# Kernel tuning notes

Measured on AMD Instinct MI355X. Metric: run time of the kernel, lower is better.

The kernel has to match this reference:

```python
import jax, jax.numpy as jnp
import numpy as np

N, IN_DIM, OUT_DIM = 8192, 512, 256
ALPHA = 0.2
NEG_INF = -9e15


def setup_inputs() -> dict:
    key = jax.random.key(0)
    k1, k2, k3, k4 = jax.random.split(key, 4)
    node_features = jax.random.normal(k1, (N, IN_DIM), dtype=jnp.float32)
    adj_matrix = jax.random.randint(k2, (N, N), 0, 2, dtype=jnp.int32)
    # xavier-uniform linear weight [out,in] -> store as [in,out]
    lim_w = float(np.sqrt(6.0 / (IN_DIM + OUT_DIM)))
    W = jax.random.uniform(k3, (IN_DIM, OUT_DIM), dtype=jnp.float32, minval=-lim_w, maxval=lim_w)
    b = jnp.zeros((OUT_DIM,), dtype=jnp.float32)
    # attention Linear(2*out_dim, 1): weight a [2*out_dim], bias scalar
    lim_a = float(np.sqrt(6.0 / (2 * OUT_DIM + 1)))
    a = jax.random.uniform(k4, (2 * OUT_DIM,), dtype=jnp.float32, minval=-lim_a, maxval=lim_a)
    a_bias = jnp.zeros((), dtype=jnp.float32)
    return {"adj_matrix": adj_matrix, "node_features": node_features, "W": W, "b": b, "a": a, "a_bias": a_bias}


def reference(adj_matrix, node_features, W, b, a, a_bias):
    # h = Linear(node_features); dropout is identity in eval mode
    h = node_features @ W + b                     # [N, D]
    # attention(cat(h_i, h_j)) == h_i @ a_l + h_j @ a_r + a_bias
    a_l, a_r = a[:OUT_DIM], a[OUT_DIM:]
    e_l = h @ a_l                                 # [N]
    e_r = h @ a_r                                 # [N]
    e = jax.nn.leaky_relu(e_l[:, None] + e_r[None, :] + a_bias, ALPHA)  # [N, N]
    scores = jnp.where(adj_matrix > 0, e, NEG_INF)
    attention = jax.nn.softmax(scores, axis=1)    # [N, N]
    h_prime = attention @ h                       # [N, D]
    return h_prime
```

## Files before the change

kernel.cpp:

```cpp
#include <hip/hip_runtime.h>

#define N 8192
#define DIN 512
#define DOUT 256
#define ALPHA 0.2f
#define NEG_INF -9.0e15f

typedef __attribute__((ext_vector_type(8))) short bf16x8;
typedef __attribute__((ext_vector_type(4))) float f32x4;
typedef __attribute__((ext_vector_type(4))) int   i32x4;

__device__ __forceinline__ unsigned f2bf_u(float f) {
    unsigned u = __builtin_bit_cast(unsigned, f);
    return (u + 0x7fffu + ((u >> 16) & 1u)) >> 16;
}
__device__ __forceinline__ unsigned pack2bf(float lo, float hi) {
    return f2bf_u(lo) | (f2bf_u(hi) << 16);
}
union U4BF8 { uint4 u; bf16x8 v; };

__device__ __forceinline__ void async_copy16(const ushort* g, ushort* l) {
    __builtin_amdgcn_global_load_lds(
        (const __attribute__((address_space(1))) unsigned*)g,
        (__attribute__((address_space(3))) unsigned*)l, 16, 0, 0);
}

__global__ __launch_bounds__(256) void wb_kernel(const float* __restrict__ W,
                                                 ushort* __restrict__ WB) {
    const int g = blockIdx.x * 256 + threadIdx.x;
    const int c = g & 255, k8 = g >> 8;
    const float* wp = W + (size_t)(k8 * 8) * DOUT + c;
    U4BF8 o;
    o.u.x = pack2bf(wp[0 * DOUT], wp[1 * DOUT]);
    o.u.y = pack2bf(wp[2 * DOUT], wp[3 * DOUT]);
    o.u.z = pack2bf(wp[4 * DOUT], wp[5 * DOUT]);
    o.u.w = pack2bf(wp[6 * DOUT], wp[7 * DOUT]);
    *(uint4*)(WB + (size_t)g * 8) = o.u;
}

__global__ __launch_bounds__(256) void h_kernel(
        const float* __restrict__ X, const ushort* __restrict__ WB,
        const float* __restrict__ bvec, const float* __restrict__ a,
        ushort* __restrict__ hB, float* __restrict__ el, float* __restrict__ er)
{
    __shared__ float red[4][64][65];
    __shared__ float elr[2][4][16];
    const int t = threadIdx.x;
    const int w = t >> 6, l = t & 63, q = l >> 4, n = l & 15;
    const int i0 = blockIdx.x * 16;
    f32x4 acc[16];
    #pragma unroll
    for (int ct = 0; ct < 16; ++ct) acc[ct] = (f32x4){0.f, 0.f, 0.f, 0.f};
    const float* xp = X + (size_t)(i0 + n) * DIN + q * 8;

    #pragma unroll
    for (int ks = 0; ks < 4; ++ks) {
        const int k0 = w * 128 + ks * 32;
        const float4 x0 = *(const float4*)(xp + k0);
        const float4 x1 = *(const float4*)(xp + k0 + 4);
        U4BF8 pa;
        pa.u.x = pack2bf(x0.x, x0.y); pa.u.y = pack2bf(x0.z, x0.w);
        pa.u.z = pack2bf(x1.x, x1.y); pa.u.w = pack2bf(x1.z, x1.w);
        const ushort* wbp = WB + ((k0 >> 3) + q) * 2048 + n * 8;
        bf16x8 bfr[16];
        #pragma unroll
        for (int ct = 0; ct < 16; ++ct) bfr[ct] = *(const bf16x8*)(wbp + ct * 128);
        #pragma unroll
        for (int ct = 0; ct < 16; ++ct)
            acc[ct] = __builtin_amdgcn_mfma_f32_16x16x32_bf16(pa.v, bfr[ct], acc[ct], 0, 0, 0);
    }
    #pragma unroll
    for (int ct = 0; ct < 16; ++ct)
        #pragma unroll
        for (int r = 0; r < 4; ++r) red[w][l][ct * 4 + r] = acc[ct][r];
    __syncthreads();

    float pl[4] = {0.f, 0.f, 0.f, 0.f}, pr[4] = {0.f, 0.f, 0.f, 0.f};
    const int hbase = (blockIdx.x * 2 + (q >> 1)) * 2048 + n * 8 + (q & 1) * 4;
    #pragma unroll
    for (int c2 = 0; c2 < 4; ++c2) {
        const int ct = w * 4 + c2;
        const float bb = bvec[ct * 16 + n];
        const float al = a[ct * 16 + n];
        const float ar = a[DOUT + ct * 16 + n];
        float v[4];
        #pragma unroll
        for (int r = 0; r < 4; ++r) {
            v[r] = red[0][l][ct * 4 + r] + red[1][l][ct * 4 + r]
                 + red[2][l][ct * 4 + r] + red[3][l][ct * 4 + r] + bb;
            pl[r] += v[r] * al;
            pr[r] += v[r] * ar;
        }
        ushort4 hp;
        hp.x = (ushort)f2bf_u(v[0]); hp.y = (ushort)f2bf_u(v[1]);
        hp.z = (ushort)f2bf_u(v[2]); hp.w = (ushort)f2bf_u(v[3]);
        *(ushort4*)&hB[hbase + ct * 128] = hp;
    }
    #pragma unroll
    for (int r = 0; r < 4; ++r) {
        #pragma unroll
        for (int off = 1; off < 16; off <<= 1) {
            pl[r] += __shfl_xor(pl[r], off);
            pr[r] += __shfl_xor(pr[r], off);
        }
    }
    if (n == 0) {
        #pragma unroll
        for (int r = 0; r < 4; ++r) {
            elr[0][w][q * 4 + r] = pl[r];
            elr[1][w][q * 4 + r] = pr[r];
        }
    }
    __syncthreads();
    if (t < 16) {
        el[i0 + t] = elr[0][0][t] + elr[0][1][t] + elr[0][2][t] + elr[0][3][t];
        er[i0 + t] = elr[1][0][t] + elr[1][1][t] + elr[1][2][t] + elr[1][3][t];
    }
}

__global__ __launch_bounds__(512, 1) void attn_kernel(
        const int* __restrict__ adj, const float* __restrict__ el,
        const float* __restrict__ er, const float* __restrict__ ab,
        const ushort* __restrict__ hB, float* __restrict__ pout,
        float* __restrict__ plsum)
{
    __shared__ ushort stage[2][32768];
    __shared__ float ers[2048];
    const int t = threadIdx.x;
    const int w = t >> 6, l = t & 63, q = l >> 4, n = l & 15;
    const int rb = blockIdx.x >> 2, jq = blockIdx.x & 3;
    const int j0 = jq * 2048;
    const int row = rb * 128 + w * 16 + n;
    const float elm = el[row] + ab[0];
    const int* alp = adj + (size_t)row * N + j0 + q * 8;

    f32x4 acc[16];
    #pragma unroll
    for (int ct = 0; ct < 16; ++ct) acc[ct] = (f32x4){0.f, 0.f, 0.f, 0.f};
    float lsum = 0.f;

    *(float4*)&ers[t * 4] = *(const float4*)&er[j0 + t * 4];
    i32x4 a[8];
    #pragma unroll
    for (int kg = 0; kg < 4; ++kg) {
        a[2 * kg]     = __builtin_nontemporal_load((const i32x4*)(alp + kg * 32));
        a[2 * kg + 1] = __builtin_nontemporal_load((const i32x4*)(alp + kg * 32 + 4));
    }
    {
        const ushort* g = hB + (size_t)j0 * 256 + t * 8;
        ushort* lb = &stage[0][t * 8];
        #pragma unroll
        for (int i = 0; i < 8; ++i) async_copy16(g + i * 4096, lb + i * 4096);
    }

    for (int s = 0; s < 16; ++s) {
        __syncthreads();
        if (s < 15) {
            const ushort* g = hB + (size_t)(j0 + (s + 1) * 128) * 256 + t * 8;
            ushort* lb = &stage[(s + 1) & 1][t * 8];
            #pragma unroll
            for (int i = 0; i < 8; ++i) async_copy16(g + i * 4096, lb + i * 4096);
        }
        U4BF8 pa[4];
        #pragma unroll
        for (int kg = 0; kg < 4; ++kg) {
            const float4 e0 = *(const float4*)&ers[s * 128 + kg * 32 + q * 8];
            const float4 e1 = *(const float4*)&ers[s * 128 + kg * 32 + q * 8 + 4];
            const i32x4 a0 = a[2 * kg], a1 = a[2 * kg + 1];
            float v, p0, p1, p2, p3, p4, p5, p6, p7;
            v = elm + e0.x; v = fmaxf(v, ALPHA * v); p0 = __expf(a0.x > 0 ? v : NEG_INF);
            v = elm + e0.y; v = fmaxf(v, ALPHA * v); p1 = __expf(a0.y > 0 ? v : NEG_INF);
            v = elm + e0.z; v = fmaxf(v, ALPHA * v); p2 = __expf(a0.z > 0 ? v : NEG_INF);
            v = elm + e0.w; v = fmaxf(v, ALPHA * v); p3 = __expf(a0.w > 0 ? v : NEG_INF);
            v = elm + e1.x; v = fmaxf(v, ALPHA * v); p4 = __expf(a1.x > 0 ? v : NEG_INF);
            v = elm + e1.y; v = fmaxf(v, ALPHA * v); p5 = __expf(a1.y > 0 ? v : NEG_INF);
            v = elm + e1.z; v = fmaxf(v, ALPHA * v); p6 = __expf(a1.z > 0 ? v : NEG_INF);
            v = elm + e1.w; v = fmaxf(v, ALPHA * v); p7 = __expf(a1.w > 0 ? v : NEG_INF);
            lsum += p0 + p1 + p2 + p3 + p4 + p5 + p6 + p7;
            pa[kg].u.x = pack2bf(p0, p1); pa[kg].u.y = pack2bf(p2, p3);
            pa[kg].u.z = pack2bf(p4, p5); pa[kg].u.w = pack2bf(p6, p7);
        }
        if (s < 15) {
            const int* ap = alp + (s + 1) * 128;
            #pragma unroll
            for (int kg = 0; kg < 4; ++kg) {
                a[2 * kg]     = __builtin_nontemporal_load((const i32x4*)(ap + kg * 32));
                a[2 * kg + 1] = __builtin_nontemporal_load((const i32x4*)(ap + kg * 32 + 4));
            }
        }
        #pragma unroll
        for (int kg = 0; kg < 4; ++kg) {
            const ushort* sb = &stage[s & 1][(kg * 4 + q) * 2048 + n * 8];
            #pragma unroll
            for (int ct = 0; ct < 16; ++ct) {
                const bf16x8 bf = *(const bf16x8*)(sb + ct * 128);
                acc[ct] = __builtin_amdgcn_mfma_f32_16x16x32_bf16(pa[kg].v, bf, acc[ct], 0, 0, 0);
            }
        }
    }

    lsum += __shfl_xor(lsum, 16);
    lsum += __shfl_xor(lsum, 32);
    if (l < 16) plsum[(size_t)jq * N + row] = lsum;

    float* pb = pout + ((size_t)jq * N + rb * 128 + w * 16 + q * 4) * 256 + n;
    #pragma unroll
    for (int ct = 0; ct < 16; ++ct)
        #pragma unroll
        for (int r = 0; r < 4; ++r)
            __builtin_nontemporal_store(acc[ct][r], pb + (size_t)r * 256 + ct * 16);
}

__global__ __launch_bounds__(256) void combine_kernel(
        const float* __restrict__ pout, const float* __restrict__ plsum,
        float* __restrict__ out)
{
    const int t = threadIdx.x;
    const int row = blockIdx.x * 4 + (t >> 6);
    const int c = (t & 63) * 4;
    const size_t idx = (size_t)row * 256 + c;
    const size_t qs = (size_t)N * 256;
    float4 v0 = *(const float4*)&pout[idx];
    float4 v1 = *(const float4*)&pout[idx + qs];
    float4 v2 = *(const float4*)&pout[idx + 2 * qs];
    float4 v3 = *(const float4*)&pout[idx + 3 * qs];
    const float li = 1.0f / (plsum[row] + plsum[N + row]
                           + plsum[2 * N + row] + plsum[3 * N + row]);
    float4 o;
    o.x = (v0.x + v1.x + v2.x + v3.x) * li;
    o.y = (v0.y + v1.y + v2.y + v3.y) * li;
    o.z = (v0.z + v1.z + v2.z + v3.z) * li;
    o.w = (v0.w + v1.w + v2.w + v3.w) * li;
    *(float4*)&out[idx] = o;
}

extern "C" void kernel_launch(void* const* d_in, const int* in_sizes, int n_in,
                              void* d_out, int out_size, void* d_ws, size_t ws_size,
                              hipStream_t stream) {
    const int*   adj = (const int*)  d_in[0];
    const float* X   = (const float*)d_in[1];
    const float* W   = (const float*)d_in[2];
    const float* b   = (const float*)d_in[3];
    const float* a   = (const float*)d_in[4];
    const float* ab  = (const float*)d_in[5];
    float* out = (float*)d_out;

    ushort* hB    = (ushort*)d_ws;
    ushort* WB    = hB + (size_t)N * DOUT;
    float*  el    = (float*)(WB + (size_t)DIN * DOUT);
    float*  er    = el + N;
    float*  plsum = er + N;
    float*  pout  = plsum + 4 * N;

    wb_kernel<<<dim3(64), dim3(256), 0, stream>>>(W, WB);
    h_kernel<<<dim3(N / 16), dim3(256), 0, stream>>>(X, WB, b, a, hB, el, er);
    attn_kernel<<<dim3(256), dim3(512), 0, stream>>>(adj, el, er, ab, hB, pout, plsum);
    combine_kernel<<<dim3(N / 4), dim3(256), 0, stream>>>(pout, plsum, out);
}
```

Baseline: 418.8 us.

## Give each wave two row tiles so B fragments are reused across MFMAs

The attention kernel now runs 256 threads (4 waves) per block instead of 512, with each wave computing 32 rows as two 16-row tiles. Each B fragment read from LDS feeds two MFMAs. The staged key tile shrinks to 64 columns per step with twice as many steps, halving shared memory so two blocks can sit on a CU. The goal is fewer LDS reads per MFMA and better latency hiding, at the cost of doubled accumulator registers, which may spill or cap occupancy, and more barriers.

```diff
diff --git a/kernel.cpp b/kernel.cpp
--- a/kernel.cpp
+++ b/kernel.cpp
@@ -118,97 +118,121 @@
     }
 }
 
-__global__ __launch_bounds__(512, 1) void attn_kernel(
+#define EXP8(ELM, E0, E1, M0, M1, PA, LS)                                          \
+    {                                                                              \
+        float v, p0, p1, p2, p3, p4, p5, p6, p7;                                   \
+        v = ELM + E0.x; v = fmaxf(v, ALPHA * v); p0 = __expf(M0.x > 0 ? v : NEG_INF); \
+        v = ELM + E0.y; v = fmaxf(v, ALPHA * v); p1 = __expf(M0.y > 0 ? v : NEG_INF); \
+        v = ELM + E0.z; v = fmaxf(v, ALPHA * v); p2 = __expf(M0.z > 0 ? v : NEG_INF); \
+        v = ELM + E0.w; v = fmaxf(v, ALPHA * v); p3 = __expf(M0.w > 0 ? v : NEG_INF); \
+        v = ELM + E1.x; v = fmaxf(v, ALPHA * v); p4 = __expf(M1.x > 0 ? v : NEG_INF); \
+        v = ELM + E1.y; v = fmaxf(v, ALPHA * v); p5 = __expf(M1.y > 0 ? v : NEG_INF); \
+        v = ELM + E1.z; v = fmaxf(v, ALPHA * v); p6 = __expf(M1.z > 0 ? v : NEG_INF); \
+        v = ELM + E1.w; v = fmaxf(v, ALPHA * v); p7 = __expf(M1.w > 0 ? v : NEG_INF); \
+        LS += p0 + p1 + p2 + p3 + p4 + p5 + p6 + p7;                               \
+        PA.u.x = pack2bf(p0, p1); PA.u.y = pack2bf(p2, p3);                        \
+        PA.u.z = pack2bf(p4, p5); PA.u.w = pack2bf(p6, p7);                        \
+    }
+
+__global__ __launch_bounds__(256, 2) void attn_kernel(
         const int* __restrict__ adj, const float* __restrict__ el,
         const float* __restrict__ er, const float* __restrict__ ab,
         const ushort* __restrict__ hB, float* __restrict__ pout,
         float* __restrict__ plsum)
 {
-    __shared__ ushort stage[2][32768];
+    __shared__ ushort stage[2][16384];
     __shared__ float ers[2048];
     const int t = threadIdx.x;
     const int w = t >> 6, l = t & 63, q = l >> 4, n = l & 15;
     const int rb = blockIdx.x >> 2, jq = blockIdx.x & 3;
     const int j0 = jq * 2048;
-    const int row = rb * 128 + w * 16 + n;
-    const float elm = el[row] + ab[0];
-    const int* alp = adj + (size_t)row * N + j0 + q * 8;
-
-    f32x4 acc[16];
-    #pragma unroll
-    for (int ct = 0; ct < 16; ++ct) acc[ct] = (f32x4){0.f, 0.f, 0.f, 0.f};
-    float lsum = 0.f;
-
-    *(float4*)&ers[t * 4] = *(const float4*)&er[j0 + t * 4];
-    i32x4 a[8];
-    #pragma unroll
-    for (int kg = 0; kg < 4; ++kg) {
-        a[2 * kg]     = __builtin_nontemporal_load((const i32x4*)(alp + kg * 32));
-        a[2 * kg + 1] = __builtin_nontemporal_load((const i32x4*)(alp + kg * 32 + 4));
+    const int row0 = rb * 128 + w * 32 + n;
+    const float elm0 = el[row0] + ab[0];
+    const float elm1 = el[row0 + 16] + ab[0];
+    const int* alp0 = adj + (size_t)row0 * N + j0 + q * 8;
+    const int* alp1 = alp0 + (size_t)16 * N;
+
+    f32x4 acc0[16], acc1[16];
+    #pragma unroll
+    for (int ct = 0; ct < 16; ++ct) {
+        acc0[ct] = (f32x4){0.f, 0.f, 0.f, 0.f};
+        acc1[ct] = (f32x4){0.f, 0.f, 0.f, 0.f};
+    }
+    float lsum0 = 0.f, lsum1 = 0.f;
+
+    *(float4*)&ers[t * 8]     = *(const float4*)&er[j0 + t * 8];
+    *(float4*)&ers[t * 8 + 4] = *(const float4*)&er[j0 + t * 8 + 4];
+    i32x4 a0[4], a1[4];
+    #pragma unroll
+    for (int kg = 0; kg < 2; ++kg) {
+        a0[2 * kg]     = __builtin_nontemporal_load((const i32x4*)(alp0 + kg * 32));
+        a0[2 * kg + 1] = __builtin_nontemporal_load((const i32x4*)(alp0 + kg * 32 + 4));
+        a1[2 * kg]     = __builtin_nontemporal_load((const i32x4*)(alp1 + kg * 32));
+        a1[2 * kg + 1] = __builtin_nontemporal_load((const i32x4*)(alp1 + kg * 32 + 4));
     }
     {
         const ushort* g = hB + (size_t)j0 * 256 + t * 8;
         ushort* lb = &stage[0][t * 8];
         #pragma unroll
-        for (int i = 0; i < 8; ++i) async_copy16(g + i * 4096, lb + i * 4096);
-    }
-
-    for (int s = 0; s < 16; ++s) {
+        for (int i = 0; i < 8; ++i) async_copy16(g + i * 2048, lb + i * 2048);
+    }
+
+    for (int s = 0; s < 32; ++s) {
         __syncthreads();
-        if (s < 15) {
-            const ushort* g = hB + (size_t)(j0 + (s + 1) * 128) * 256 + t * 8;
+        if (s < 31) {
+            const ushort* g = hB + (size_t)(j0 + (s + 1) * 64) * 256 + t * 8;
             ushort* lb = &stage[(s + 1) & 1][t * 8];
             #pragma unroll
-            for (int i = 0; i < 8; ++i) async_copy16(g + i * 4096, lb + i * 4096);
-        }
-        U4BF8 pa[4];
-        #pragma unroll
-        for (int kg = 0; kg < 4; ++kg) {
-            const float4 e0 = *(const float4*)&ers[s * 128 + kg * 32 + q * 8];
-            const float4 e1 = *(const float4*)&ers[s * 128 + kg * 32 + q * 8 + 4];
-            const i32x4 a0 = a[2 * kg], a1 = a[2 * kg + 1];
-            float v, p0, p1, p2, p3, p4, p5, p6, p7;
-            v = elm + e0.x; v = fmaxf(v, ALPHA * v); p0 = __expf(a0.x > 0 ? v : NEG_INF);
-            v = elm + e0.y; v = fmaxf(v, ALPHA * v); p1 = __expf(a0.y > 0 ? v : NEG_INF);
-            v = elm + e0.z; v = fmaxf(v, ALPHA * v); p2 = __expf(a0.z > 0 ? v : NEG_INF);
-            v = elm + e0.w; v = fmaxf(v, ALPHA * v); p3 = __expf(a0.w > 0 ? v : NEG_INF);
-            v = elm + e1.x; v = fmaxf(v, ALPHA * v); p4 = __expf(a1.x > 0 ? v : NEG_INF);
-            v = elm + e1.y; v = fmaxf(v, ALPHA * v); p5 = __expf(a1.y > 0 ? v : NEG_INF);
-            v = elm + e1.z; v = fmaxf(v, ALPHA * v); p6 = __expf(a1.z > 0 ? v : NEG_INF);
-            v = elm + e1.w; v = fmaxf(v, ALPHA * v); p7 = __expf(a1.w > 0 ? v : NEG_INF);
-            lsum += p0 + p1 + p2 + p3 + p4 + p5 + p6 + p7;
-            pa[kg].u.x = pack2bf(p0, p1); pa[kg].u.y = pack2bf(p2, p3);
-            pa[kg].u.z = pack2bf(p4, p5); pa[kg].u.w = pack2bf(p6, p7);
-        }
-        if (s < 15) {
-            const int* ap = alp + (s + 1) * 128;
+            for (int i = 0; i < 8; ++i) async_copy16(g + i * 2048, lb + i * 2048);
+        }
+        U4BF8 pa0[2], pa1[2];
+        #pragma unroll
+        for (int kg = 0; kg < 2; ++kg) {
+            const float4 e0 = *(const float4*)&ers[s * 64 + kg * 32 + q * 8];
+            const float4 e1 = *(const float4*)&ers[s * 64 + kg * 32 + q * 8 + 4];
+            const i32x4 m00 = a0[2 * kg], m01 = a0[2 * kg + 1];
+            const i32x4 m10 = a1[2 * kg], m11 = a1[2 * kg + 1];
+            EXP8(elm0, e0, e1, m00, m01, pa0[kg], lsum0);
+            EXP8(elm1, e0, e1, m10, m11, pa1[kg], lsum1);
+        }
+        if (s < 31) {
+            const int* ap0 = alp0 + (s + 1) * 64;
+            const int* ap1 = alp1 + (s + 1) * 64;
             #pragma unroll
-            for (int kg = 0; kg < 4; ++kg) {
-                a[2 * kg]     = __builtin_nontemporal_load((const i32x4*)(ap + kg * 32));
-                a[2 * kg + 1] = __builtin_nontemporal_load((const i32x4*)(ap + kg * 32 + 4));
+            for (int kg = 0; kg < 2; ++kg) {
+                a0[2 * kg]     = __builtin_nontemporal_load((const i32x4*)(ap0 + kg * 32));
+                a0[2 * kg + 1] = __builtin_nontemporal_load((const i32x4*)(ap0 + kg * 32 + 4));
+                a1[2 * kg]     = __builtin_nontemporal_load((const i32x4*)(ap1 + kg * 32));
+                a1[2 * kg + 1] = __builtin_nontemporal_load((const i32x4*)(ap1 + kg * 32 + 4));
             }
         }
         #pragma unroll
-        for (int kg = 0; kg < 4; ++kg) {
+        for (int kg = 0; kg < 2; ++kg) {
             const ushort* sb = &stage[s & 1][(kg * 4 + q) * 2048 + n * 8];
             #pragma unroll
             for (int ct = 0; ct < 16; ++ct) {
                 const bf16x8 bf = *(const bf16x8*)(sb + ct * 128);
-                acc[ct] = __builtin_amdgcn_mfma_f32_16x16x32_bf16(pa[kg].v, bf, acc[ct], 0, 0, 0);
+                acc0[ct] = __builtin_amdgcn_mfma_f32_16x16x32_bf16(pa0[kg].v, bf, acc0[ct], 0, 0, 0);
+                acc1[ct] = __builtin_amdgcn_mfma_f32_16x16x32_bf16(pa1[kg].v, bf, acc1[ct], 0, 0, 0);
             }
         }
     }
 
-    lsum += __shfl_xor(lsum, 16);
-    lsum += __shfl_xor(lsum, 32);
-    if (l < 16) plsum[(size_t)jq * N + row] = lsum;
-
-    float* pb = pout + ((size_t)jq * N + rb * 128 + w * 16 + q * 4) * 256 + n;
+    lsum0 += __shfl_xor(lsum0, 16); lsum0 += __shfl_xor(lsum0, 32);
+    lsum1 += __shfl_xor(lsum1, 16); lsum1 += __shfl_xor(lsum1, 32);
+    if (l < 16) {
+        plsum[(size_t)jq * N + rb * 128 + w * 32 + l]      = lsum0;
+        plsum[(size_t)jq * N + rb * 128 + w * 32 + 16 + l] = lsum1;
+    }
+
+    float* pb = pout + ((size_t)jq * N + rb * 128 + w * 32 + q * 4) * 256 + n;
     #pragma unroll
     for (int ct = 0; ct < 16; ++ct)
         #pragma unroll
-        for (int r = 0; r < 4; ++r)
-            __builtin_nontemporal_store(acc[ct][r], pb + (size_t)r * 256 + ct * 16);
+        for (int r = 0; r < 4; ++r) {
+            __builtin_nontemporal_store(acc0[ct][r], pb + (size_t)r * 256 + ct * 16);
+            __builtin_nontemporal_store(acc1[ct][r], pb + (size_t)(16 + r) * 256 + ct * 16);
+        }
 }
 
 __global__ __launch_bounds__(256) void combine_kernel(
@@ -254,6 +278,6 @@
 
     wb_kernel<<<dim3(64), dim3(256), 0, stream>>>(W, WB);
     h_kernel<<<dim3(N / 16), dim3(256), 0, stream>>>(X, WB, b, a, hB, el, er);
-    attn_kernel<<<dim3(256), dim3(512), 0, stream>>>(adj, el, er, ab, hB, pout, plsum);
+    attn_kernel<<<dim3(256), dim3(256), 0, stream>>>(adj, el, er, ab, hB, pout, plsum);
     combine_kernel<<<dim3(N / 4), dim3(256), 0, stream>>>(pout, plsum, out);
 }
```

Measured after the change: 436.7 us. 1.04x slower.

## Switch attention to 32x32 MFMA with split-K waves and register double-buffered adjacency

Applied to the files above, without the earlier changes.

The attention kernel moves from 16x16x32 to 32x32x16 bf16 MFMA. Each pair of waves now splits the K range of a 32-row group, and the two partial accumulators are reduced through LDS at the end. Adjacency loads are double-buffered in two register sets with explicit vmcnt waits, and sched barriers order the loop. Launch bounds ask for 2 blocks per CU to raise occupancy. The LDS reduction and split lsum add some cost, and the higher occupancy target may cause register spills.

```diff
diff --git a/kernel.cpp b/kernel.cpp
--- a/kernel.cpp
+++ b/kernel.cpp
@@ -8,6 +8,7 @@
 
 typedef __attribute__((ext_vector_type(8))) short bf16x8;
 typedef __attribute__((ext_vector_type(4))) float f32x4;
+typedef __attribute__((ext_vector_type(16))) float f32x16;
 typedef __attribute__((ext_vector_type(4))) int   i32x4;
 
 __device__ __forceinline__ unsigned f2bf_u(float f) {
@@ -118,7 +119,63 @@
     }
 }
 
-__global__ __launch_bounds__(512, 1) void attn_kernel(
+#define EXP8(ELM, E0, E1, M0, M1, PA, LS)                                          \
+    {                                                                              \
+        float v, p0, p1, p2, p3, p4, p5, p6, p7;                                   \
+        v = ELM + E0.x; v = fmaxf(v, ALPHA * v); p0 = __expf(M0.x > 0 ? v : NEG_INF); \
+        v = ELM + E0.y; v = fmaxf(v, ALPHA * v); p1 = __expf(M0.y > 0 ? v : NEG_INF); \
+        v = ELM + E0.z; v = fmaxf(v, ALPHA * v); p2 = __expf(M0.z > 0 ? v : NEG_INF); \
+        v = ELM + E0.w; v = fmaxf(v, ALPHA * v); p3 = __expf(M0.w > 0 ? v : NEG_INF); \
+        v = ELM + E1.x; v = fmaxf(v, ALPHA * v); p4 = __expf(M1.x > 0 ? v : NEG_INF); \
+        v = ELM + E1.y; v = fmaxf(v, ALPHA * v); p5 = __expf(M1.y > 0 ? v : NEG_INF); \
+        v = ELM + E1.z; v = fmaxf(v, ALPHA * v); p6 = __expf(M1.z > 0 ? v : NEG_INF); \
+        v = ELM + E1.w; v = fmaxf(v, ALPHA * v); p7 = __expf(M1.w > 0 ? v : NEG_INF); \
+        LS += p0 + p1 + p2 + p3 + p4 + p5 + p6 + p7;                               \
+        PA.u.x = pack2bf(p0, p1); PA.u.y = pack2bf(p2, p3);                        \
+        PA.u.z = pack2bf(p4, p5); PA.u.w = pack2bf(p6, p7);                        \
+    }
+
+#define ATTN_STEP(S, CUR, NXT)                                                        \
+    {                                                                                 \
+        const int s_ = (S);                                                           \
+        if (s_ < 15) {                             \
+            const ushort* g = hB + (size_t)(j0 + (s_ + 1) * 128) * 256 + t * 8;       \
+            ushort* lb = &stage[(s_ + 1) & 1][t * 8];                                 \
+            _Pragma("unroll")                                                         \
+            for (int i = 0; i < 8; ++i) async_copy16(g + i * 4096, lb + i * 4096);    \
+        }                                                                             \
+        __builtin_amdgcn_sched_barrier(0);                                            \
+        if (s_ < 15) {                             \
+            const int* ap = alp + (s_ + 1) * 128;                                     \
+            _Pragma("unroll")                                                         \
+            for (int ks = 0; ks < 4; ++ks) {                                          \
+                NXT[2 * ks]     = __builtin_nontemporal_load((const i32x4*)(ap + ks * 16));     \
+                NXT[2 * ks + 1] = __builtin_nontemporal_load((const i32x4*)(ap + ks * 16 + 4)); \
+            }                                                                         \
+        }                                                                             \
+        __builtin_amdgcn_sched_barrier(0);                                            \
+        _Pragma("unroll")                                                             \
+        for (int ks = 0; ks < 4; ++ks) {                                              \
+            const float4 e0 = *(const float4*)&ers[s_ * 128 + kh * 64 + ks * 16 + hi * 8];     \
+            const float4 e1 = *(const float4*)&ers[s_ * 128 + kh * 64 + ks * 16 + hi * 8 + 4]; \
+            U4BF8 pa;                                                                 \
+            EXP8(elm, e0, e1, CUR[2 * ks], CUR[2 * ks + 1], pa, lsum);                \
+            const ushort* sb = &stage[s_ & 1][(kh * 8 + ks * 2 + hi) * 2048 + r32 * 8];        \
+            _Pragma("unroll")                                                         \
+            for (int ct = 0; ct < 8; ++ct) {                                          \
+                const bf16x8 bf = *(const bf16x8*)(sb + ct * 256);                    \
+                acc[ct] = __builtin_amdgcn_mfma_f32_32x32x16_bf16(pa.v, bf, acc[ct], 0, 0, 0); \
+            }                                                                         \
+        }                                                                             \
+        if (s_ < 15) {                                                                \
+            asm volatile("s_waitcnt vmcnt(8)" ::: "memory");       \
+            __builtin_amdgcn_sched_barrier(0);                                        \
+            __builtin_amdgcn_s_barrier();                                             \
+            __builtin_amdgcn_sched_barrier(0);                                        \
+        }                                                                             \
+    }
+
+__global__ __launch_bounds__(512, 2) void attn_kernel(
         const int* __restrict__ adj, const float* __restrict__ el,
         const float* __restrict__ er, const float* __restrict__ ab,
         const ushort* __restrict__ hB, float* __restrict__ pout,
@@ -126,25 +183,30 @@
 {
     __shared__ ushort stage[2][32768];
     __shared__ float ers[2048];
+    __shared__ float lsum_lds[8][32];
     const int t = threadIdx.x;
-    const int w = t >> 6, l = t & 63, q = l >> 4, n = l & 15;
+    const int w = t >> 6, l = t & 63;
+    const int rg = w & 3, kh = w >> 2;
+    const int r32 = l & 31, hi = l >> 5;
     const int rb = blockIdx.x >> 2, jq = blockIdx.x & 3;
     const int j0 = jq * 2048;
-    const int row = rb * 128 + w * 16 + n;
+    const int row = rb * 128 + rg * 32 + r32;
     const float elm = el[row] + ab[0];
-    const int* alp = adj + (size_t)row * N + j0 + q * 8;
-
-    f32x4 acc[16];
-    #pragma unroll
-    for (int ct = 0; ct < 16; ++ct) acc[ct] = (f32x4){0.f, 0.f, 0.f, 0.f};
+    const int* alp = adj + (size_t)row * N + j0 + kh * 64 + hi * 8;
+
+    f32x16 acc[8];
+    #pragma unroll
+    for (int ct = 0; ct < 8; ++ct)
+        #pragma unroll
+        for (int r = 0; r < 16; ++r) acc[ct][r] = 0.f;
     float lsum = 0.f;
 
     *(float4*)&ers[t * 4] = *(const float4*)&er[j0 + t * 4];
-    i32x4 a[8];
-    #pragma unroll
-    for (int kg = 0; kg < 4; ++kg) {
-        a[2 * kg]     = __builtin_nontemporal_load((const i32x4*)(alp + kg * 32));
-        a[2 * kg + 1] = __builtin_nontemporal_load((const i32x4*)(alp + kg * 32 + 4));
+    i32x4 aA[8], aB[8];
+    #pragma unroll
+    for (int ks = 0; ks < 4; ++ks) {
+        aA[2 * ks]     = __builtin_nontemporal_load((const i32x4*)(alp + ks * 16));
+        aA[2 * ks + 1] = __builtin_nontemporal_load((const i32x4*)(alp + ks * 16 + 4));
     }
     {
         const ushort* g = hB + (size_t)j0 * 256 + t * 8;
@@ -152,63 +214,52 @@
         #pragma unroll
         for (int i = 0; i < 8; ++i) async_copy16(g + i * 4096, lb + i * 4096);
     }
-
-    for (int s = 0; s < 16; ++s) {
-        __syncthreads();
-        if (s < 15) {
-            const ushort* g = hB + (size_t)(j0 + (s + 1) * 128) * 256 + t * 8;
-            ushort* lb = &stage[(s + 1) & 1][t * 8];
+    __syncthreads();
+
+    for (int s2 = 0; s2 < 8; ++s2) {
+        ATTN_STEP(2 * s2,     aA, aB);
+        ATTN_STEP(2 * s2 + 1, aB, aA);
+    }
+
+    lsum += __shfl_xor(lsum, 32);
+    if (l < 32) lsum_lds[w][l] = lsum;
+    __syncthreads();
+
+    if (kh == 1) {
+        float* dst = (float*)stage + rg * 8192 + l * 16;
+        #pragma unroll
+        for (int ct = 0; ct < 8; ++ct) {
+            *(float4*)&dst[ct * 1024 + 0]  = make_float4(acc[ct][0],  acc[ct][1],  acc[ct][2],  acc[ct][3]);
+            *(float4*)&dst[ct * 1024 + 4]  = make_float4(acc[ct][4],  acc[ct][5],  acc[ct][6],  acc[ct][7]);
+            *(float4*)&dst[ct * 1024 + 8]  = make_float4(acc[ct][8],  acc[ct][9],  acc[ct][10], acc[ct][11]);
+            *(float4*)&dst[ct * 1024 + 12] = make_float4(acc[ct][12], acc[ct][13], acc[ct][14], acc[ct][15]);
+        }
+    }
+    __syncthreads();
+    if (kh == 0) {
+        const float* src = (const float*)stage + rg * 8192 + l * 16;
+        #pragma unroll
+        for (int ct = 0; ct < 8; ++ct)
             #pragma unroll
-            for (int i = 0; i < 8; ++i) async_copy16(g + i * 4096, lb + i * 4096);
-        }
-        U4BF8 pa[4];
-        #pragma unroll
-        for (int kg = 0; kg < 4; ++kg) {
-            const float4 e0 = *(const float4*)&ers[s * 128 + kg * 32 + q * 8];
-            const float4 e1 = *(const float4*)&ers[s * 128 + kg * 32 + q * 8 + 4];
-            const i32x4 a0 = a[2 * kg], a1 = a[2 * kg + 1];
-            float v, p0, p1, p2, p3, p4, p5, p6, p7;
-            v = elm + e0.x; v = fmaxf(v, ALPHA * v); p0 = __expf(a0.x > 0 ? v : NEG_INF);
-            v = elm + e0.y; v = fmaxf(v, ALPHA * v); p1 = __expf(a0.y > 0 ? v : NEG_INF);
-            v = elm + e0.z; v = fmaxf(v, ALPHA * v); p2 = __expf(a0.z > 0 ? v : NEG_INF);
-            v = elm + e0.w; v = fmaxf(v, ALPHA * v); p3 = __expf(a0.w > 0 ? v : NEG_INF);
-            v = elm + e1.x; v = fmaxf(v, ALPHA * v); p4 = __expf(a1.x > 0 ? v : NEG_INF);
-            v = elm + e1.y; v = fmaxf(v, ALPHA * v); p5 = __expf(a1.y > 0 ? v : NEG_INF);
-            v = elm + e1.z; v = fmaxf(v, ALPHA * v); p6 = __expf(a1.z > 0 ? v : NEG_INF);
-            v = elm + e1.w; v = fmaxf(v, ALPHA * v); p7 = __expf(a1.w > 0 ? v : NEG_INF);
-            lsum += p0 + p1 + p2 + p3 + p4 + p5 + p6 + p7;
-            pa[kg].u.x = pack2bf(p0, p1); pa[kg].u.y = pack2bf(p2, p3);
-            pa[kg].u.z = pack2bf(p4, p5); pa[kg].u.w = pack2bf(p6, p7);
-        }
-        if (s < 15) {
-            const int* ap = alp + (s + 1) * 128;
+            for (int g4 = 0; g4 < 4; ++g4) {
+                const float4 o = *(const float4*)&src[ct * 1024 + g4 * 4];
+                acc[ct][g4 * 4 + 0] += o.x;
+                acc[ct][g4 * 4 + 1] += o.y;
+                acc[ct][g4 * 4 + 2] += o.z;
+                acc[ct][g4 * 4 + 3] += o.w;
+            }
+        if (l < 32)
+            plsum[(size_t)jq * N + rb * 128 + rg * 32 + l] =
+                lsum_lds[rg][l] + lsum_lds[rg + 4][l];
+        float* pb = pout + ((size_t)jq * N + rb * 128 + rg * 32) * 256 + r32;
+        #pragma unroll
+        for (int ct = 0; ct < 8; ++ct)
             #pragma unroll
-            for (int kg = 0; kg < 4; ++kg) {
-                a[2 * kg]     = __builtin_nontemporal_load((const i32x4*)(ap + kg * 32));
-                a[2 * kg + 1] = __builtin_nontemporal_load((const i32x4*)(ap + kg * 32 + 4));
+            for (int r = 0; r < 16; ++r) {
+                const int rl = (r & 3) + 8 * (r >> 2) + 4 * hi;
+                __builtin_nontemporal_store(acc[ct][r], pb + (size_t)rl * 256 + ct * 32);
             }
-        }
-        #pragma unroll
-        for (int kg = 0; kg < 4; ++kg) {
-            const ushort* sb = &stage[s & 1][(kg * 4 + q) * 2048 + n * 8];
-            #pragma unroll
-            for (int ct = 0; ct < 16; ++ct) {
-                const bf16x8 bf = *(const bf16x8*)(sb + ct * 128);
-                acc[ct] = __builtin_amdgcn_mfma_f32_16x16x32_bf16(pa[kg].v, bf, acc[ct], 0, 0, 0);
-            }
-        }
-    }
-
-    lsum += __shfl_xor(lsum, 16);
-    lsum += __shfl_xor(lsum, 32);
-    if (l < 16) plsum[(size_t)jq * N + row] = lsum;
-
-    float* pb = pout + ((size_t)jq * N + rb * 128 + w * 16 + q * 4) * 256 + n;
-    #pragma unroll
-    for (int ct = 0; ct < 16; ++ct)
-        #pragma unroll
-        for (int r = 0; r < 4; ++r)
-            __builtin_nontemporal_store(acc[ct][r], pb + (size_t)r * 256 + ct * 16);
+    }
 }
 
 __global__ __launch_bounds__(256) void combine_kernel(
```

New measurement: 445.0 us. 1.06x slower.

## Switch attention kernel to 32x32x16 MFMA with column-split waves

Applied to the files above, without the earlier changes.

Reworks the attention matmul from 16x16x32 MFMA to 32x32x16 MFMA. Each wave now owns 32 rows and half of the 256 output columns, so two waves share a row group and each recomputes the exponentials for its rows. The adjacency prefetch is split into two half-tile register sets reloaded between the halves. Launch bounds are relaxed to allow two blocks per CU, and the adjacency loads are no longer nontemporal. The aim is fewer LDS B-fragment reads per FLOP and better MFMA efficiency, paid for with duplicated exp/mask work across wave pairs.

```diff
diff --git a/kernel.cpp b/kernel.cpp
--- a/kernel.cpp
+++ b/kernel.cpp
@@ -8,6 +8,7 @@
 
 typedef __attribute__((ext_vector_type(8))) short bf16x8;
 typedef __attribute__((ext_vector_type(4))) float f32x4;
+typedef __attribute__((ext_vector_type(16))) float f32x16;
 typedef __attribute__((ext_vector_type(4))) int   i32x4;
 
 __device__ __forceinline__ unsigned f2bf_u(float f) {
@@ -118,7 +119,23 @@
     }
 }
 
-__global__ __launch_bounds__(512, 1) void attn_kernel(
+#define EXP8(ELM, E0, E1, M0, M1, PA, LS)                                          \
+    {                                                                              \
+        float v, p0, p1, p2, p3, p4, p5, p6, p7;                                   \
+        v = ELM + E0.x; v = fmaxf(v, ALPHA * v); p0 = __expf(M0.x > 0 ? v : NEG_INF); \
+        v = ELM + E0.y; v = fmaxf(v, ALPHA * v); p1 = __expf(M0.y > 0 ? v : NEG_INF); \
+        v = ELM + E0.z; v = fmaxf(v, ALPHA * v); p2 = __expf(M0.z > 0 ? v : NEG_INF); \
+        v = ELM + E0.w; v = fmaxf(v, ALPHA * v); p3 = __expf(M0.w > 0 ? v : NEG_INF); \
+        v = ELM + E1.x; v = fmaxf(v, ALPHA * v); p4 = __expf(M1.x > 0 ? v : NEG_INF); \
+        v = ELM + E1.y; v = fmaxf(v, ALPHA * v); p5 = __expf(M1.y > 0 ? v : NEG_INF); \
+        v = ELM + E1.z; v = fmaxf(v, ALPHA * v); p6 = __expf(M1.z > 0 ? v : NEG_INF); \
+        v = ELM + E1.w; v = fmaxf(v, ALPHA * v); p7 = __expf(M1.w > 0 ? v : NEG_INF); \
+        LS += p0 + p1 + p2 + p3 + p4 + p5 + p6 + p7;                               \
+        PA.u.x = pack2bf(p0, p1); PA.u.y = pack2bf(p2, p3);                        \
+        PA.u.z = pack2bf(p4, p5); PA.u.w = pack2bf(p6, p7);                        \
+    }
+
+__global__ __launch_bounds__(512, 2) void attn_kernel(
         const int* __restrict__ adj, const float* __restrict__ el,
         const float* __restrict__ er, const float* __restrict__ ab,
         const ushort* __restrict__ hB, float* __restrict__ pout,
@@ -127,24 +144,30 @@
     __shared__ ushort stage[2][32768];
     __shared__ float ers[2048];
     const int t = threadIdx.x;
-    const int w = t >> 6, l = t & 63, q = l >> 4, n = l & 15;
+    const int w = t >> 6, l = t & 63;
+    const int rg = w >> 1, ch = w & 1;
+    const int r32 = l & 31, hi = l >> 5;
     const int rb = blockIdx.x >> 2, jq = blockIdx.x & 3;
     const int j0 = jq * 2048;
-    const int row = rb * 128 + w * 16 + n;
+    const int row = rb * 128 + rg * 32 + r32;
     const float elm = el[row] + ab[0];
-    const int* alp = adj + (size_t)row * N + j0 + q * 8;
-
-    f32x4 acc[16];
-    #pragma unroll
-    for (int ct = 0; ct < 16; ++ct) acc[ct] = (f32x4){0.f, 0.f, 0.f, 0.f};
+    const int* alp = adj + (size_t)row * N + j0 + hi * 8;
+
+    f32x16 acc[4];
+    #pragma unroll
+    for (int ct = 0; ct < 4; ++ct)
+        #pragma unroll
+        for (int r = 0; r < 16; ++r) acc[ct][r] = 0.f;
     float lsum = 0.f;
 
     *(float4*)&ers[t * 4] = *(const float4*)&er[j0 + t * 4];
-    i32x4 a[8];
-    #pragma unroll
-    for (int kg = 0; kg < 4; ++kg) {
-        a[2 * kg]     = __builtin_nontemporal_load((const i32x4*)(alp + kg * 32));
-        a[2 * kg + 1] = __builtin_nontemporal_load((const i32x4*)(alp + kg * 32 + 4));
+    i32x4 adjA[8], adjB[8];
+    #pragma unroll
+    for (int ks = 0; ks < 4; ++ks) {
+        adjA[2 * ks]     = *(const i32x4*)(alp + ks * 16);
+        adjA[2 * ks + 1] = *(const i32x4*)(alp + ks * 16 + 4);
+        adjB[2 * ks]     = *(const i32x4*)(alp + 64 + ks * 16);
+        adjB[2 * ks + 1] = *(const i32x4*)(alp + 64 + ks * 16 + 4);
     }
     {
         const ushort* g = hB + (size_t)j0 * 256 + t * 8;
@@ -161,54 +184,63 @@
             #pragma unroll
             for (int i = 0; i < 8; ++i) async_copy16(g + i * 4096, lb + i * 4096);
         }
-        U4BF8 pa[4];
-        #pragma unroll
-        for (int kg = 0; kg < 4; ++kg) {
-            const float4 e0 = *(const float4*)&ers[s * 128 + kg * 32 + q * 8];
-            const float4 e1 = *(const float4*)&ers[s * 128 + kg * 32 + q * 8 + 4];
-            const i32x4 a0 = a[2 * kg], a1 = a[2 * kg + 1];
-            float v, p0, p1, p2, p3, p4, p5, p6, p7;
-            v = elm + e0.x; v = fmaxf(v, ALPHA * v); p0 = __expf(a0.x > 0 ? v : NEG_INF);
-            v = elm + e0.y; v = fmaxf(v, ALPHA * v); p1 = __expf(a0.y > 0 ? v : NEG_INF);
-            v = elm + e0.z; v = fmaxf(v, ALPHA * v); p2 = __expf(a0.z > 0 ? v : NEG_INF);
-            v = elm + e0.w; v = fmaxf(v, ALPHA * v); p3 = __expf(a0.w > 0 ? v : NEG_INF);
-            v = elm + e1.x; v = fmaxf(v, ALPHA * v); p4 = __expf(a1.x > 0 ? v : NEG_INF);
-            v = elm + e1.y; v = fmaxf(v, ALPHA * v); p5 = __expf(a1.y > 0 ? v : NEG_INF);
-            v = elm + e1.z; v = fmaxf(v, ALPHA * v); p6 = __expf(a1.z > 0 ? v : NEG_INF);
-            v = elm + e1.w; v = fmaxf(v, ALPHA * v); p7 = __expf(a1.w > 0 ? v : NEG_INF);
-            lsum += p0 + p1 + p2 + p3 + p4 + p5 + p6 + p7;
-            pa[kg].u.x = pack2bf(p0, p1); pa[kg].u.y = pack2bf(p2, p3);
-            pa[kg].u.z = pack2bf(p4, p5); pa[kg].u.w = pack2bf(p6, p7);
+        const ushort* sbase = &stage[s & 1][ch * 1024 + r32 * 8];
+        #pragma unroll
+        for (int ks = 0; ks < 4; ++ks) {
+            const float4 e0 = *(const float4*)&ers[s * 128 + ks * 16 + hi * 8];
+            const float4 e1 = *(const float4*)&ers[s * 128 + ks * 16 + hi * 8 + 4];
+            U4BF8 pa;
+            EXP8(elm, e0, e1, adjA[2 * ks], adjA[2 * ks + 1], pa, lsum);
+            const ushort* sb = sbase + (ks * 2 + hi) * 2048;
+            #pragma unroll
+            for (int ct = 0; ct < 4; ++ct) {
+                const bf16x8 bf = *(const bf16x8*)(sb + ct * 256);
+                acc[ct] = __builtin_amdgcn_mfma_f32_32x32x16_bf16(pa.v, bf, acc[ct], 0, 0, 0);
+            }
         }
         if (s < 15) {
             const int* ap = alp + (s + 1) * 128;
             #pragma unroll
-            for (int kg = 0; kg < 4; ++kg) {
-                a[2 * kg]     = __builtin_nontemporal_load((const i32x4*)(ap + kg * 32));
-                a[2 * kg + 1] = __builtin_nontemporal_load((const i32x4*)(ap + kg * 32 + 4));
-            }
-        }
-        #pragma unroll
-        for (int kg = 0; kg < 4; ++kg) {
-            const ushort* sb = &stage[s & 1][(kg * 4 + q) * 2048 + n * 8];
-            #pragma unroll
-            for (int ct = 0; ct < 16; ++ct) {
-                const bf16x8 bf = *(const bf16x8*)(sb + ct * 128);
-                acc[ct] = __builtin_amdgcn_mfma_f32_16x16x32_bf16(pa[kg].v, bf, acc[ct], 0, 0, 0);
-            }
-        }
-    }
-
-    lsum += __shfl_xor(lsum, 16);
+            for (int ks = 0; ks < 4; ++ks) {
+                adjA[2 * ks]     = *(const i32x4*)(ap + ks * 16);
+                adjA[2 * ks + 1] = *(const i32x4*)(ap + ks * 16 + 4);
+            }
+        }
+        #pragma unroll
+        for (int ks = 0; ks < 4; ++ks) {
+            const float4 e0 = *(const float4*)&ers[s * 128 + 64 + ks * 16 + hi * 8];
+            const float4 e1 = *(const float4*)&ers[s * 128 + 64 + ks * 16 + hi * 8 + 4];
+            U4BF8 pa;
+            EXP8(elm, e0, e1, adjB[2 * ks], adjB[2 * ks + 1], pa, lsum);
+            const ushort* sb = sbase + (8 + ks * 2 + hi) * 2048;
+            #pragma unroll
+            for (int ct = 0; ct < 4; ++ct) {
+                const bf16x8 bf = *(const bf16x8*)(sb + ct * 256);
+                acc[ct] = __builtin_amdgcn_mfma_f32_32x32x16_bf16(pa.v, bf, acc[ct], 0, 0, 0);
+            }
+        }
+        if (s < 15) {
+            const int* ap = alp + (s + 1) * 128 + 64;
+            #pragma unroll
+            for (int ks = 0; ks < 4; ++ks) {
+                adjB[2 * ks]     = *(const i32x4*)(ap + ks * 16);
+                adjB[2 * ks + 1] = *(const i32x4*)(ap + ks * 16 + 4);
+            }
+        }
+    }
+
     lsum += __shfl_xor(lsum, 32);
-    if (l < 16) plsum[(size_t)jq * N + row] = lsum;
-
-    float* pb = pout + ((size_t)jq * N + rb * 128 + w * 16 + q * 4) * 256 + n;
-    #pragma unroll
-    for (int ct = 0; ct < 16; ++ct)
-        #pragma unroll
-        for (int r = 0; r < 4; ++r)
-            __builtin_nontemporal_store(acc[ct][r], pb + (size_t)r * 256 + ct * 16);
+    if (ch == 0 && l < 32)
+        plsum[(size_t)jq * N + rb * 128 + rg * 32 + l] = lsum;
+
+    float* pb = pout + ((size_t)jq * N + rb * 128 + rg * 32) * 256 + ch * 128 + r32;
+    #pragma unroll
+    for (int ct = 0; ct < 4; ++ct)
+        #pragma unroll
+        for (int r = 0; r < 16; ++r) {
+            const int rl = (r & 3) + 8 * (r >> 2) + 4 * hi;
+            __builtin_nontemporal_store(acc[ct][r], pb + (size_t)rl * 256 + ct * 32);
+        }
 }
 
 __global__ __launch_bounds__(256) void combine_kernel(
```

After: 452.0 us. 1.08x slower.
